# Optimization experiments

Hardware: AMD Instinct MI355X
Metric: run time of the kernel (lower is better)

The kernel has to match this reference:

```python
import jax, jax.numpy as jnp
import numpy as np

LAYERS, HIDDEN, FFN, HEADS = 2, 128, 256, 4
IMG_H, IMG_W = 32, 64
SEQ = IMG_H * IMG_W
HEAD = HIDDEN // HEADS          # 32, per-head qk dim
HEAD_V = 2 * HEAD               # double_v_dim=True
VDIM = HEADS * HEAD_V           # 256
B = 2
SCALE_BASE = 512.0
EPS = 1e-5


def _xpos_tables(seq, d):
    # XPOS: rotary angles + per-position exponential scale
    half = d // 2
    scale_vec = (jnp.arange(0, d, 2, dtype=jnp.float32) + 0.4 * d) / (1.4 * d)  # (d/2,)
    power = jnp.arange(seq, dtype=jnp.float32) / SCALE_BASE
    scale = scale_vec[None, :] ** power[:, None]                                 # (S, d/2)
    inv_freq = 1.0 / (10000.0 ** (jnp.arange(half, dtype=jnp.float32) / half))
    ang = jnp.arange(seq, dtype=jnp.float32)[:, None] * inv_freq[None, :]        # (S, d/2)
    return jnp.sin(ang), jnp.cos(ang), scale


def _apply_xpos(x, sin, cos, scale):
    # duplicate-interleave sin/cos*scale to width d, rotate-every-two
    s = jnp.repeat(sin * scale, 2, axis=-1)   # (S, d)
    c = jnp.repeat(cos * scale, 2, axis=-1)
    x1, x2 = x[..., ::2], x[..., 1::2]
    rot = jnp.stack([-x2, x1], axis=-1).reshape(x.shape)
    return x * c + rot * s


def _ln(x, g, b):
    mu = x.mean(-1, keepdims=True)
    var = ((x - mu) ** 2).mean(-1, keepdims=True)
    return (x - mu) * jax.lax.rsqrt(var + EPS) * g + b


def _gn(y, g, b):
    # GroupNorm(HEADS groups) over VDIM channels, applied per token
    bsz, s, v = y.shape
    yg = y.reshape(bsz, s, HEADS, HEAD_V)
    mu = yg.mean(-1, keepdims=True)
    var = ((yg - mu) ** 2).mean(-1, keepdims=True)
    yn = ((yg - mu) * jax.lax.rsqrt(var + EPS)).reshape(bsz, s, v)
    return yn * g + b


def _decay(seq):
    # D[h, n, m] = gamma_h^(n-m) for n >= m else 0
    gammas = 1.0 - jnp.exp(jnp.linspace(jnp.log(1.0 / 32.0), jnp.log(1.0 / 512.0), HEADS))
    n = jnp.arange(seq, dtype=jnp.float32)
    diff = n[:, None] - n[None, :]
    return (gammas[:, None, None] ** jnp.maximum(diff, 0.0)) * (diff >= 0.0)


def _forward(x, ln1_g, ln1_b, ln2_g, ln2_b, WQ, WK, WV, WG, WO, gn_g, gn_b, w1, b1, w2, b2):
    sin, cos, scale = _xpos_tables(SEQ, HEAD)
    D = _decay(SEQ)  # (H, S, S)
    for i in range(LAYERS):
        h = _ln(x, ln1_g[i], ln1_b[i])
        Q = _apply_xpos(jnp.einsum('bsd,hde->bhse', h, WQ[i]), sin, cos, scale)
        K = _apply_xpos(jnp.einsum('bsd,hde->bhse', h, WK[i]), sin, cos, 1.0 / scale)
        V = jnp.einsum('bsd,hdv->bhsv', h, WV[i])
        att = jnp.einsum('bhse,bhte->bhst', Q, K) * D[None]      # decay retention
        Y = jnp.einsum('bhst,bhtv->bhsv', att, V)
        Y = jnp.moveaxis(Y, 1, 2).reshape(x.shape[0], SEQ, VDIM)  # concat heads
        Y = _gn(Y, gn_g[i], gn_b[i])
        G = h @ WG[i]
        ret = (G * jax.nn.sigmoid(G) * Y) @ WO[i]                 # swish gate + out proj
        y = ret + x
        h2 = _ln(y, ln2_g[i], ln2_b[i])
        x = jax.nn.gelu(h2 @ w1[i] + b1[i], approximate=False) @ w2[i] + b2[i] + y
    return x.reshape(x.shape[0], IMG_H, IMG_W, x.shape[-1])


def setup_inputs() -> dict:
    key = jax.random.key(0)
    ks = jax.random.split(key, 8)
    def rn(k, shape, sc):
        return jax.random.normal(k, shape, dtype=jnp.float32) * sc
    s = 1.0 / np.sqrt(HIDDEN)
    return {
        'x': rn(ks[0], (B, SEQ, HIDDEN), 1.0),
        'ln1_g': jnp.ones((LAYERS, HIDDEN), jnp.float32),
        'ln1_b': jnp.zeros((LAYERS, HIDDEN), jnp.float32),
        'ln2_g': jnp.ones((LAYERS, HIDDEN), jnp.float32),
        'ln2_b': jnp.zeros((LAYERS, HIDDEN), jnp.float32),
        'WQ': rn(ks[1], (LAYERS, HEADS, HIDDEN, HEAD), s),
        'WK': rn(ks[2], (LAYERS, HEADS, HIDDEN, HEAD), s),
        'WV': rn(ks[3], (LAYERS, HEADS, HIDDEN, HEAD_V), s),
        'WG': rn(ks[4], (LAYERS, HIDDEN, VDIM), s),
        'WO': rn(ks[5], (LAYERS, VDIM, HIDDEN), 1.0 / np.sqrt(VDIM)),
        'gn_g': jnp.ones((LAYERS, VDIM), jnp.float32),
        'gn_b': jnp.zeros((LAYERS, VDIM), jnp.float32),
        'w1': rn(ks[6], (LAYERS, HIDDEN, FFN), s),
        'b1': jnp.zeros((LAYERS, FFN), jnp.float32),
        'w2': rn(ks[7], (LAYERS, FFN, HIDDEN), 1.0 / np.sqrt(FFN)),
        'b2': jnp.zeros((LAYERS, HIDDEN), jnp.float32),
    }


def reference(x, ln1_g, ln1_b, ln2_g, ln2_b, WQ, WK, WV, WG, WO, gn_g, gn_b, w1, b1, w2, b2):
    return _forward(x, ln1_g, ln1_b, ln2_g, ln2_b, WQ, WK, WV, WG, WO, gn_g, gn_b, w1, b1, w2, b2)
```

## Files before the change

kernel.cpp:

```cpp
#include <hip/hip_runtime.h>
#include <math.h>

#define NLAYERS 2
#define HID 128
#define FFND 256
#define NH 4
#define SEQL 2048
#define HD 32
#define HDV 64
#define VD 256
#define NBATCH 2
#define MROWS (NBATCH*SEQL)
#define NCAT 768
#define NCHUNK 32

__global__ __launch_bounds__(256) void setup_kernel(
    const float* __restrict__ WQ, const float* __restrict__ WK,
    const float* __restrict__ WV, const float* __restrict__ WG,
    float* __restrict__ Wcat, float* __restrict__ tabs)
{
  int bid = blockIdx.x;
  if (bid < 768) {
    int idx = bid * 256 + threadIdx.x;
    int l = idx / (HID * NCAT);
    int r = idx - l * (HID * NCAT);
    int k = r / NCAT;
    int n = r - k * NCAT;
    float v;
    if (n < 128)      { int h = n >> 5, e = n & 31;            v = WQ[(((l*NH+h)*HID)+k)*HD  + e]; }
    else if (n < 256) { int m = n-128; int h = m>>5, e = m&31; v = WK[(((l*NH+h)*HID)+k)*HD  + e]; }
    else if (n < 512) { int m = n-256; int h = m>>6, e = m&63; v = WV[(((l*NH+h)*HID)+k)*HDV + e]; }
    else              { v = WG[(l*HID + k)*VD + (n-512)]; }
    Wcat[idx] = v;
  } else {
    int idx = (bid - 768) * 256 + threadIdx.x;
    int s = idx >> 4, i = idx & 15;
    float inv_freq = powf(10000.f, -(float)i * (1.f/16.f));
    float ang = (float)s * inv_freq;
    float sv  = ((float)(2*i) + 0.4f*32.f) / (1.4f*32.f);
    float sc  = powf(sv, (float)s * (1.f/512.f));
    float sn = sinf(ang), cs = cosf(ang);
    tabs[idx]          = sn * sc;
    tabs[32768 + idx]  = cs * sc;
    tabs[65536 + idx]  = sn / sc;
    tabs[98304 + idx]  = cs / sc;
  }
}

template<bool XPOS, bool BIAS, bool GELU>
__global__ __launch_bounds__(512) void gemm_ln(
    const float* __restrict__ A, const float* __restrict__ Bw,
    const float* __restrict__ lng, const float* __restrict__ lnb,
    const float* __restrict__ bias, const float* __restrict__ tabs,
    float* __restrict__ C, int N)
{
  __shared__ float As[128][68];
  __shared__ float Bs[64][68];
  int tid = threadIdx.x;
  int tx2 = tid & 31, ty2 = tid >> 5;
  int rb = blockIdx.x * 64, nb = blockIdx.y * 64;

  {
    int row = tid >> 3, q = tid & 7;
    const float* ar = A + (size_t)(rb + row) * HID + 16 * q;
    float4 av[4];
    #pragma unroll
    for (int it = 0; it < 4; it++) av[it] = *(const float4*)(ar + 4*it);
    float s = 0.f;
    #pragma unroll
    for (int it = 0; it < 4; it++) s += av[it].x + av[it].y + av[it].z + av[it].w;
    s += __shfl_xor(s, 1); s += __shfl_xor(s, 2); s += __shfl_xor(s, 4);
    float mu = s * (1.f/128.f);
    float qs = 0.f;
    #pragma unroll
    for (int it = 0; it < 4; it++) {
      float d;
      d = av[it].x - mu; qs += d*d;  d = av[it].y - mu; qs += d*d;
      d = av[it].z - mu; qs += d*d;  d = av[it].w - mu; qs += d*d;
    }
    qs += __shfl_xor(qs, 1); qs += __shfl_xor(qs, 2); qs += __shfl_xor(qs, 4);
    float rs = rsqrtf(qs * (1.f/128.f) + 1e-5f);
    #pragma unroll
    for (int it = 0; it < 4; it++) {
      int k0 = 16*q + 4*it;
      float4 g4 = *(const float4*)(lng + k0);
      float4 b4 = *(const float4*)(lnb + k0);
      float vv[4] = { (av[it].x-mu)*rs*g4.x + b4.x, (av[it].y-mu)*rs*g4.y + b4.y,
                      (av[it].z-mu)*rs*g4.z + b4.z, (av[it].w-mu)*rs*g4.w + b4.w };
      #pragma unroll
      for (int d = 0; d < 4; d++) {
        int k = k0 + d;
        As[k][row ^ (4*((k>>2)&7)) ^ (16*((k>>5)&1))] = vv[d];
      }
    }
  }

  float acc[4][2];
  #pragma unroll
  for (int i=0;i<4;i++) { acc[i][0] = 0.f; acc[i][1] = 0.f; }

  for (int ks = 0; ks < 128; ks += 64) {
    #pragma unroll
    for (int it = 0; it < 2; it++) {
      int idx = it*512 + tid;
      int kk = idx >> 4, nq = idx & 15;
      *(float4*)(&Bs[kk][4*nq]) = *(const float4*)(Bw + (size_t)(ks+kk)*N + nb + 4*nq);
    }
    __syncthreads();
    #pragma unroll
    for (int kk = 0; kk < 64; kk++) {
      int k = ks + kk;
      float a[4];
      *(float4*)a = *(const float4*)&As[k][(4*ty2) ^ (4*((k>>2)&7)) ^ (16*((k>>5)&1))];
      float2 b2 = *(const float2*)&Bs[kk][2*tx2];
      #pragma unroll
      for (int i=0;i<4;i++) {
        acc[i][0] = fmaf(a[i], b2.x, acc[i][0]);
        acc[i][1] = fmaf(a[i], b2.y, acc[i][1]);
      }
    }
    __syncthreads();
  }

  #pragma unroll
  for (int i=0;i<4;i++) {
    int row = rb + 4*ty2 + i;
    int cb = nb + 2*tx2;
    float o[2];
    #pragma unroll
    for (int j=0;j<2;j++) {
      float v = acc[i][j];
      if (BIAS)  v += bias[cb + j];
      if (GELU)  v = 0.5f * v * (1.f + erff(v * 0.70710678118f));
      o[j] = v;
    }
    if (XPOS) {
      if (nb < 256) {
        bool isK = (nb >= 128);
        const float* sn_t = tabs + (isK ? 65536 : 0);
        const float* cs_t = tabs + (isK ? 98304 : 32768);
        int s = row & (SEQL - 1);
        int i0 = (cb & 31) >> 1;
        float sn = sn_t[s*16 + i0], cs = cs_t[s*16 + i0];
        float x1 = o[0], x2 = o[1];
        o[0] = x1*cs - x2*sn;  o[1] = x2*cs + x1*sn;
      }
    }
    *(float2*)(C + (size_t)row*N + cb) = *(float2*)o;
  }
}

template<bool BIAS>
__global__ __launch_bounds__(512) void gemm_n32(
    const float* __restrict__ A, const float* __restrict__ Bw,
    const float* __restrict__ bias, const float* __restrict__ Rsd,
    float* __restrict__ C, int N)
{
  __shared__ float As[64][68];
  __shared__ float Bs[64][36];
  int tid = threadIdx.x;
  int tx = tid & 15, ty = tid >> 4;
  int rb = blockIdx.x * 64, nb = blockIdx.y * 32;

  float acc[2][2];
  acc[0][0]=0.f; acc[0][1]=0.f; acc[1][0]=0.f; acc[1][1]=0.f;

  for (int ks = 0; ks < 256; ks += 64) {
    #pragma unroll
    for (int it = 0; it < 2; it++) {
      int idx = it*512 + tid;
      int row = idx >> 4, kq = idx & 15;
      float4 a4 = *(const float4*)(A + (size_t)(rb+row)*256 + ks + 4*kq);
      int rsw = row ^ (4*(kq & 7));
      As[4*kq+0][rsw] = a4.x; As[4*kq+1][rsw] = a4.y;
      As[4*kq+2][rsw] = a4.z; As[4*kq+3][rsw] = a4.w;
    }
    {
      int kk = tid >> 3, nq = tid & 7;
      *(float4*)(&Bs[kk][4*nq]) = *(const float4*)(Bw + (size_t)(ks+kk)*N + nb + 4*nq);
    }
    __syncthreads();
    #pragma unroll
    for (int k = 0; k < 64; k++) {
      float2 a2 = *(const float2*)&As[k][(2*ty) ^ (4*((k>>2)&7))];
      float2 b2 = *(const float2*)&Bs[k][2*tx];
      acc[0][0] = fmaf(a2.x, b2.x, acc[0][0]);
      acc[0][1] = fmaf(a2.x, b2.y, acc[0][1]);
      acc[1][0] = fmaf(a2.y, b2.x, acc[1][0]);
      acc[1][1] = fmaf(a2.y, b2.y, acc[1][1]);
    }
    __syncthreads();
  }

  #pragma unroll
  for (int i=0;i<2;i++) {
    int row = rb + 2*ty + i;
    int cb = nb + 2*tx;
    float o[2];
    #pragma unroll
    for (int j=0;j<2;j++) {
      float v = acc[i][j];
      if (BIAS) v += bias[cb + j];
      v += Rsd[(size_t)row*N + cb + j];
      o[j] = v;
    }
    *(float2*)(C + (size_t)row*N + cb) = *(float2*)o;
  }
}

__global__ __launch_bounds__(512) void ret_kv_kernel(
    const float* __restrict__ QKVG, float* __restrict__ Asum)
{
  int bh = blockIdx.x >> 5;
  int c  = blockIdx.x & 31;
  int b = bh >> 2, h = bh & 3;
  float t0 = logf(1.f/32.f) + (float)h * (logf(1.f/512.f) - logf(1.f/32.f)) * (1.f/3.f);
  float gamma = 1.f - expf(t0);
  float lg = logf(gamma);

  __shared__ float Ks[64][36];
  __shared__ float Vs[64][68];
  __shared__ float wt[64];

  int tid = threadIdx.x;
  int c0 = c * 64;
  const float* base = QKVG + (size_t)(b * SEQL) * NCAT;

  {
    int row = tid >> 3, eq = tid & 7;
    *(float4*)&Ks[row][4*eq] =
        *(const float4*)(base + (size_t)(c0+row)*NCAT + 128 + h*32 + 4*eq);
  }
  #pragma unroll
  for (int it = 0; it < 2; it++) {
    int idx = it*512 + tid;
    int row = idx >> 4, vq = idx & 15;
    *(float4*)&Vs[row][4*vq] =
        *(const float4*)(base + (size_t)(c0+row)*NCAT + 256 + h*64 + 4*vq);
  }
  if (tid < 64) wt[tid] = __expf(lg * (float)(64 - tid));
  __syncthreads();

  int e = tid >> 4, v4 = (tid & 15) * 4;
  float a0[4] = {0,0,0,0};
  #pragma unroll 8
  for (int t = 0; t < 64; t++) {
    float kw = Ks[t][e] * wt[t];
    float4 v0 = *(const float4*)&Vs[t][v4];
    a0[0] = fmaf(kw, v0.x, a0[0]); a0[1] = fmaf(kw, v0.y, a0[1]);
    a0[2] = fmaf(kw, v0.z, a0[2]); a0[3] = fmaf(kw, v0.w, a0[3]);
  }
  *(float4*)(Asum + ((size_t)(bh*NCHUNK + c))*2048 + e*64 + v4) = *(float4*)a0;
}

__global__ __launch_bounds__(512) void ret_out_kernel(
    const float* __restrict__ QKVG, const float* __restrict__ Asum,
    const float* __restrict__ gn_g, const float* __restrict__ gn_b,
    float* __restrict__ Gated)
{
  int bh = blockIdx.x >> 5;
  int c  = blockIdx.x & 31;
  int b = bh >> 2, h = bh & 3;
  float t0 = logf(1.f/32.f) + (float)h * (logf(1.f/512.f) - logf(1.f/32.f)) * (1.f/3.f);
  float gamma = 1.f - expf(t0);
  float lg = logf(gamma);
  float g64 = __expf(lg * 64.f);

  __shared__ float Qs[64][36];
  __shared__ float Ks[64][36];
  __shared__ float Vs[64][68];
  __shared__ float Ss[64][68];
  __shared__ float Sc[32][68];

  int tid = threadIdx.x;
  int tx2 = tid & 31, ty2 = tid >> 5;
  int c0 = c * 64;
  const float* base = QKVG + (size_t)(b * SEQL) * NCAT;

  {
    int row = tid >> 3, eq = tid & 7;
    *(float4*)&Qs[row][4*eq] =
        *(const float4*)(base + (size_t)(c0+row)*NCAT + h*32 + 4*eq);
    int esw = (4*eq) ^ (4*((row >> 2) & 7));
    *(float4*)&Ks[row][esw] =
        *(const float4*)(base + (size_t)(c0+row)*NCAT + 128 + h*32 + 4*eq);
  }
  #pragma unroll
  for (int it = 0; it < 2; it++) {
    int idx = it*512 + tid;
    int row = idx >> 4, vq = idx & 15;
    *(float4*)&Vs[row][4*vq] =
        *(const float4*)(base + (size_t)(c0+row)*NCAT + 256 + h*64 + 4*vq);
  }

  {
    int e = tid >> 4, v4 = (tid & 15) * 4;
    float s0[4] = {0,0,0,0};
    float w = 1.f;
    const float* ab = Asum + ((size_t)bh*NCHUNK)*2048 + e*64 + v4;
    for (int cp = c-1; cp >= 0; --cp) {
      const float* ap = ab + (size_t)cp*2048;
      float4 x0 = *(const float4*)ap;
      s0[0] = fmaf(w, x0.x, s0[0]); s0[1] = fmaf(w, x0.y, s0[1]);
      s0[2] = fmaf(w, x0.z, s0[2]); s0[3] = fmaf(w, x0.w, s0[3]);
      w *= g64;
    }
    *(float4*)&Sc[e][v4] = *(float4*)s0;
  }
  __syncthreads();

  float sacc[4][2];
  #pragma unroll
  for (int i=0;i<4;i++) { sacc[i][0]=0.f; sacc[i][1]=0.f; }
  #pragma unroll
  for (int e = 0; e < 32; e += 4) {
    float qv[4][4], kv[2][4];
    #pragma unroll
    for (int i=0;i<4;i++)
      *(float4*)qv[i] = *(const float4*)&Qs[4*ty2+i][e];
    #pragma unroll
    for (int j=0;j<2;j++) {
      int kr = 2*tx2 + j;
      *(float4*)kv[j] = *(const float4*)&Ks[kr][e ^ (4*((kr>>2)&7))];
    }
    #pragma unroll
    for (int i=0;i<4;i++)
      #pragma unroll
      for (int j=0;j<2;j++)
        sacc[i][j] = fmaf(qv[i][0], kv[j][0],
                     fmaf(qv[i][1], kv[j][1],
                     fmaf(qv[i][2], kv[j][2],
                     fmaf(qv[i][3], kv[j][3], sacc[i][j]))));
  }
  #pragma unroll
  for (int i=0;i<4;i++) {
    int sl = 4*ty2 + i;
    float o2[2];
    #pragma unroll
    for (int j=0;j<2;j++) {
      int dr = sl - (2*tx2 + j);
      float w = (dr >= 0) ? __expf(lg * (float)dr) : 0.f;
      o2[j] = sacc[i][j] * w;
    }
    *(float2*)&Ss[sl][2*tx2] = *(float2*)o2;
  }

  float acc[4][2];
  #pragma unroll
  for (int i=0;i<4;i++) { acc[i][0]=0.f; acc[i][1]=0.f; }
  #pragma unroll
  for (int e = 0; e < 32; e += 4) {
    float qv[4][4], sv[4][2];
    #pragma unroll
    for (int i=0;i<4;i++)
      *(float4*)qv[i] = *(const float4*)&Qs[4*ty2+i][e];
    #pragma unroll
    for (int m=0;m<4;m++)
      *(float2*)sv[m] = *(const float2*)&Sc[e+m][2*tx2];
    #pragma unroll
    for (int i=0;i<4;i++)
      #pragma unroll
      for (int j=0;j<2;j++)
        acc[i][j] = fmaf(qv[i][0], sv[0][j],
                    fmaf(qv[i][1], sv[1][j],
                    fmaf(qv[i][2], sv[2][j],
                    fmaf(qv[i][3], sv[3][j], acc[i][j]))));
  }
  #pragma unroll
  for (int i=0;i<4;i++) {
    float gr = __expf(lg * (float)(4*ty2 + i));
    acc[i][0] *= gr; acc[i][1] *= gr;
  }
  __syncthreads();

  #pragma unroll
  for (int t = 0; t < 64; t += 4) {
    float sv[4][4], vv[4][2];
    #pragma unroll
    for (int i=0;i<4;i++)
      *(float4*)sv[i] = *(const float4*)&Ss[4*ty2+i][t];
    #pragma unroll
    for (int m=0;m<4;m++)
      *(float2*)vv[m] = *(const float2*)&Vs[t+m][2*tx2];
    #pragma unroll
    for (int i=0;i<4;i++)
      #pragma unroll
      for (int j=0;j<2;j++)
        acc[i][j] = fmaf(sv[i][0], vv[0][j],
                    fmaf(sv[i][1], vv[1][j],
                    fmaf(sv[i][2], vv[2][j],
                    fmaf(sv[i][3], vv[3][j], acc[i][j]))));
  }

  #pragma unroll
  for (int i=0;i<4;i++) {
    float s1 = acc[i][0] + acc[i][1];
    #pragma unroll
    for (int o = 16; o; o >>= 1) s1 += __shfl_xor(s1, o);
    float mu = s1 * (1.f/64.f);
    float q = 0.f;
    #pragma unroll
    for (int j=0;j<2;j++) { float d = acc[i][j] - mu; q += d*d; }
    #pragma unroll
    for (int o = 16; o; o >>= 1) q += __shfl_xor(q, o);
    float rs = rsqrtf(q * (1.f/64.f) + 1e-5f);
    int row = b*SEQL + c0 + 4*ty2 + i;
    float2 g2 = *(const float2*)(QKVG + (size_t)row*NCAT + 512 + h*64 + 2*tx2);
    float gv[2] = {g2.x, g2.y};
    float o2[2];
    #pragma unroll
    for (int j=0;j<2;j++) {
      int col = h*64 + 2*tx2 + j;
      float yn = (acc[i][j] - mu) * rs * gn_g[col] + gn_b[col];
      float g = gv[j];
      float sig = 1.f / (1.f + __expf(-g));
      o2[j] = g * sig * yn;
    }
    *(float2*)(Gated + (size_t)row*VD + h*64 + 2*tx2) = *(float2*)o2;
  }
}

extern "C" void kernel_launch(void* const* d_in, const int* in_sizes, int n_in,
                              void* d_out, int out_size, void* d_ws, size_t ws_size,
                              hipStream_t stream)
{
  (void)in_sizes; (void)n_in; (void)out_size; (void)ws_size;
  const float* x_in  = (const float*)d_in[0];
  const float* ln1_g = (const float*)d_in[1];
  const float* ln1_b = (const float*)d_in[2];
  const float* ln2_g = (const float*)d_in[3];
  const float* ln2_b = (const float*)d_in[4];
  const float* WQ    = (const float*)d_in[5];
  const float* WK    = (const float*)d_in[6];
  const float* WV    = (const float*)d_in[7];
  const float* WG    = (const float*)d_in[8];
  const float* WO    = (const float*)d_in[9];
  const float* gn_g  = (const float*)d_in[10];
  const float* gn_b  = (const float*)d_in[11];
  const float* w1    = (const float*)d_in[12];
  const float* b1    = (const float*)d_in[13];
  const float* w2    = (const float*)d_in[14];
  const float* b2    = (const float*)d_in[15];
  float* out = (float*)d_out;
  float* ws  = (float*)d_ws;

  float* Wcat = ws;
  float* tabs = Wcat + 196608;
  float* QKVG = tabs + 131072;
  float* Asum = QKVG + 3145728;
  float* Gt   = Asum + 524288;
  float* Yres = Gt   + 1048576;
  float* Mid  = Yres + 524288;

  setup_kernel<<<896, 256, 0, stream>>>(WQ, WK, WV, WG, Wcat, tabs);

  for (int l = 0; l < NLAYERS; l++) {
    const float* xl = (l == 0) ? x_in : out;
    gemm_ln<true,false,false><<<dim3(MROWS/64, NCAT/64), 512, 0, stream>>>(
        xl, Wcat + l*HID*NCAT, ln1_g + l*HID, ln1_b + l*HID,
        nullptr, tabs, QKVG, NCAT);
    ret_kv_kernel<<<256, 512, 0, stream>>>(QKVG, Asum);
    ret_out_kernel<<<256, 512, 0, stream>>>(QKVG, Asum, gn_g + l*VD, gn_b + l*VD, Gt);
    gemm_n32<false><<<dim3(MROWS/64, HID/32), 512, 0, stream>>>(
        Gt, WO + l*VD*HID, nullptr, xl, Yres, HID);
    gemm_ln<false,true,true><<<dim3(MROWS/64, FFND/64), 512, 0, stream>>>(
        Yres, w1 + l*HID*FFND, ln2_g + l*HID, ln2_b + l*HID,
        b1 + l*FFND, nullptr, Mid, FFND);
    gemm_n32<true><<<dim3(MROWS/64, HID/32), 512, 0, stream>>>(
        Mid, w2 + l*FFND*HID, b2 + l*HID, Yres, out, HID);
  }
}
```

Before: 232.5 us.

## Fuse LN+QKVG projection with chunk KV state and fuse whole FFN block

Replaces the setup kernel, the LN+QKVG GEMM and the separate KV-state kernel with one kernel. It reads the weights directly, computes the xPos tables inline, and emits partial per-16-row KV sums that ret_out now adds up four at a time. The WO projection, residual add, LN2, W1 with GELU, W2 and the second residual are merged into a single kernel over 16-row tiles. This cuts kernel launches from 13 to 6 and avoids round trips through global memory for intermediates. In exchange, each block reads the weights directly from global memory with no shared-memory tiling, and only 256 blocks are launched.

Measured after the change: 287.5 us. +23.6%, slower.

```diff
diff --git a/kernel.cpp b/kernel.cpp
--- a/kernel.cpp
+++ b/kernel.cpp
@@ -14,256 +14,180 @@
 #define NCAT 768
 #define NCHUNK 32
 
-__global__ __launch_bounds__(256) void setup_kernel(
+#define LG32   (-3.4657359028f)
+#define DLT    (-0.9241962407f)
+__device__ __forceinline__ float lgamma_h(int h) {
+  return logf(1.f - expf(LG32 + DLT * (float)h));
+}
+
+__global__ __launch_bounds__(512) void fuse_qkvg(
+    const float* __restrict__ X,
+    const float* __restrict__ lng, const float* __restrict__ lnb,
     const float* __restrict__ WQ, const float* __restrict__ WK,
     const float* __restrict__ WV, const float* __restrict__ WG,
-    float* __restrict__ Wcat, float* __restrict__ tabs)
+    float* __restrict__ QKVG, float* __restrict__ Asum4, int l)
 {
-  int bid = blockIdx.x;
-  if (bid < 768) {
-    int idx = bid * 256 + threadIdx.x;
-    int l = idx / (HID * NCAT);
-    int r = idx - l * (HID * NCAT);
-    int k = r / NCAT;
-    int n = r - k * NCAT;
-    float v;
-    if (n < 128)      { int h = n >> 5, e = n & 31;            v = WQ[(((l*NH+h)*HID)+k)*HD  + e]; }
-    else if (n < 256) { int m = n-128; int h = m>>5, e = m&31; v = WK[(((l*NH+h)*HID)+k)*HD  + e]; }
-    else if (n < 512) { int m = n-256; int h = m>>6, e = m&63; v = WV[(((l*NH+h)*HID)+k)*HDV + e]; }
-    else              { v = WG[(l*HID + k)*VD + (n-512)]; }
-    Wcat[idx] = v;
-  } else {
-    int idx = (bid - 768) * 256 + threadIdx.x;
-    int s = idx >> 4, i = idx & 15;
-    float inv_freq = powf(10000.f, -(float)i * (1.f/16.f));
-    float ang = (float)s * inv_freq;
-    float sv  = ((float)(2*i) + 0.4f*32.f) / (1.4f*32.f);
-    float sc  = powf(sv, (float)s * (1.f/512.f));
-    float sn = sinf(ang), cs = cosf(ang);
-    tabs[idx]          = sn * sc;
-    tabs[32768 + idx]  = cs * sc;
-    tabs[65536 + idx]  = sn / sc;
-    tabs[98304 + idx]  = cs / sc;
+  __shared__ union {
+    float As[128][20];
+    struct { float wK[16][132]; float Vl[16][260]; } kv;
+  } sm;
+
+  int tid = threadIdx.x;
+  int rb = blockIdx.x * 16;
+  int ty = tid >> 6;
+  int tx = tid & 63;
+
+  {
+    int row = tid >> 5, q = tid & 31;
+    float4 av = *(const float4*)(X + (size_t)(rb + row) * HID + 4*q);
+    float s = av.x + av.y + av.z + av.w;
+    s += __shfl_xor(s, 1);  s += __shfl_xor(s, 2);
+    s += __shfl_xor(s, 4);  s += __shfl_xor(s, 8);  s += __shfl_xor(s, 16);
+    float mu = s * (1.f/128.f);
+    float dx = av.x-mu, dy = av.y-mu, dz = av.z-mu, dw = av.w-mu;
+    float qs = dx*dx + dy*dy + dz*dz + dw*dw;
+    qs += __shfl_xor(qs, 1);  qs += __shfl_xor(qs, 2);
+    qs += __shfl_xor(qs, 4);  qs += __shfl_xor(qs, 8);  qs += __shfl_xor(qs, 16);
+    float rs = rsqrtf(qs * (1.f/128.f) + 1e-5f);
+    float4 g4 = *(const float4*)(lng + 4*q);
+    float4 b4 = *(const float4*)(lnb + 4*q);
+    sm.As[4*q+0][row] = dx*rs*g4.x + b4.x;
+    sm.As[4*q+1][row] = dy*rs*g4.y + b4.y;
+    sm.As[4*q+2][row] = dz*rs*g4.z + b4.z;
+    sm.As[4*q+3][row] = dw*rs*g4.w + b4.w;
+  }
+
+  bool isK = (tx >= 32);
+  int txk = isK ? (tx - 32) : tx;
+  int cq  = 4 * txk;
+  const float* b0 = (isK ? WK : WQ) + (size_t)l*NH*HID*HD
+                    + (txk >> 3) * (HID*HD) + (cq & 31);
+  const float* b1 = WV + (size_t)l*NH*HID*HDV
+                    + (tx >> 4) * (HID*HDV) + ((4*tx) & 63);
+  const float* b2 = WG + (size_t)l*HID*VD + 4*tx;
+
+  __syncthreads();
+
+  float acc[2][12];
+  #pragma unroll
+  for (int i=0;i<2;i++)
+    #pragma unroll
+    for (int j=0;j<12;j++) acc[i][j] = 0.f;
+
+  #pragma unroll 4
+  for (int k = 0; k < 128; k++) {
+    float2 a = *(const float2*)&sm.As[k][2*ty];
+    float4 q0 = *(const float4*)(b0 + k*HD);
+    float4 v0 = *(const float4*)(b1 + k*HDV);
+    float4 g0 = *(const float4*)(b2 + k*VD);
+    float bv[12] = { q0.x,q0.y,q0.z,q0.w, v0.x,v0.y,v0.z,v0.w, g0.x,g0.y,g0.z,g0.w };
+    float ar[2] = { a.x, a.y };
+    #pragma unroll
+    for (int i=0;i<2;i++)
+      #pragma unroll
+      for (int j=0;j<12;j++)
+        acc[i][j] = fmaf(ar[i], bv[j], acc[i][j]);
+  }
+
+  {
+    float sgn = isK ? -1.f : 1.f;
+    #pragma unroll
+    for (int P = 0; P < 2; P++) {
+      float fi   = (float)(((cq & 31) >> 1) + P);
+      float invf = exp2f(fi * -0.83048202372f);
+      float sv   = (2.f*fi + 12.8f) * (1.f/44.8f);
+      float l2sv = log2f(sv) * (1.f/512.f) * sgn;
+      #pragma unroll
+      for (int i=0;i<2;i++) {
+        float s  = (float)((rb & (SEQL-1)) + 2*ty + i);
+        float ang = s * invf;
+        float sc  = exp2f(l2sv * s);
+        float sn = sinf(ang) * sc, cs = cosf(ang) * sc;
+        float x1 = acc[i][2*P], x2 = acc[i][2*P+1];
+        acc[i][2*P]   = x1*cs - x2*sn;
+        acc[i][2*P+1] = x2*cs + x1*sn;
+      }
+    }
+  }
+
+  #pragma unroll
+  for (int i=0;i<2;i++) {
+    float* cp = QKVG + (size_t)(rb + 2*ty + i) * NCAT;
+    float o0[4] = {acc[i][0],acc[i][1],acc[i][2],acc[i][3]};
+    float o1[4] = {acc[i][4],acc[i][5],acc[i][6],acc[i][7]};
+    float o2[4] = {acc[i][8],acc[i][9],acc[i][10],acc[i][11]};
+    *(float4*)(cp + 4*tx)       = *(float4*)o0;
+    *(float4*)(cp + 256 + 4*tx) = *(float4*)o1;
+    *(float4*)(cp + 512 + 4*tx) = *(float4*)o2;
+  }
+
+  __syncthreads();
+
+  if (isK) {
+    float lgk = lgamma_h(cq >> 5);
+    #pragma unroll
+    for (int i=0;i<2;i++) {
+      int t = 2*ty + i;
+      float w = expf(lgk * (float)(16 - t));
+      float o[4] = {acc[i][0]*w, acc[i][1]*w, acc[i][2]*w, acc[i][3]*w};
+      *(float4*)&sm.kv.wK[t][cq] = *(float4*)o;
+    }
+  }
+  #pragma unroll
+  for (int i=0;i<2;i++) {
+    float o[4] = {acc[i][4],acc[i][5],acc[i][6],acc[i][7]};
+    *(float4*)&sm.kv.Vl[2*ty+i][4*tx] = *(float4*)o;
+  }
+  __syncthreads();
+
+  {
+    int h  = tid >> 7;
+    int u  = tid & 127;
+    int e2 = u >> 3;
+    int v8 = u & 7;
+    float pa[2][8];
+    #pragma unroll
+    for (int i=0;i<2;i++)
+      #pragma unroll
+      for (int j=0;j<8;j++) pa[i][j] = 0.f;
+    #pragma unroll
+    for (int t = 0; t < 16; t++) {
+      float2 ke = *(const float2*)&sm.kv.wK[t][h*32 + 2*e2];
+      float4 va = *(const float4*)&sm.kv.Vl[t][h*64 + 8*v8];
+      float4 vb = *(const float4*)&sm.kv.Vl[t][h*64 + 8*v8 + 4];
+      float vv[8] = {va.x,va.y,va.z,va.w, vb.x,vb.y,vb.z,vb.w};
+      float kk[2] = {ke.x, ke.y};
+      #pragma unroll
+      for (int i=0;i<2;i++)
+        #pragma unroll
+        for (int j=0;j<8;j++)
+          pa[i][j] = fmaf(kk[i], vv[j], pa[i][j]);
+    }
+    int b = rb >> 11;
+    int c = (rb & (SEQL-1)) >> 6;
+    int p = (rb >> 4) & 3;
+    float scale = expf(lgamma_h(h) * (float)(48 - 16*p));
+    float* ob = Asum4 + ((size_t)((b*NH + h)*NCHUNK + c)*4 + p)*2048
+                + (2*e2)*64 + 8*v8;
+    #pragma unroll
+    for (int i=0;i<2;i++) {
+      float o0[4] = {pa[i][0]*scale, pa[i][1]*scale, pa[i][2]*scale, pa[i][3]*scale};
+      float o1[4] = {pa[i][4]*scale, pa[i][5]*scale, pa[i][6]*scale, pa[i][7]*scale};
+      *(float4*)(ob + i*64)     = *(float4*)o0;
+      *(float4*)(ob + i*64 + 4) = *(float4*)o1;
+    }
   }
 }
 
-template<bool XPOS, bool BIAS, bool GELU>
-__global__ __launch_bounds__(512) void gemm_ln(
-    const float* __restrict__ A, const float* __restrict__ Bw,
-    const float* __restrict__ lng, const float* __restrict__ lnb,
-    const float* __restrict__ bias, const float* __restrict__ tabs,
-    float* __restrict__ C, int N)
-{
-  __shared__ float As[128][68];
-  __shared__ float Bs[64][68];
-  int tid = threadIdx.x;
-  int tx2 = tid & 31, ty2 = tid >> 5;
-  int rb = blockIdx.x * 64, nb = blockIdx.y * 64;
-
-  {
-    int row = tid >> 3, q = tid & 7;
-    const float* ar = A + (size_t)(rb + row) * HID + 16 * q;
-    float4 av[4];
-    #pragma unroll
-    for (int it = 0; it < 4; it++) av[it] = *(const float4*)(ar + 4*it);
-    float s = 0.f;
-    #pragma unroll
-    for (int it = 0; it < 4; it++) s += av[it].x + av[it].y + av[it].z + av[it].w;
-    s += __shfl_xor(s, 1); s += __shfl_xor(s, 2); s += __shfl_xor(s, 4);
-    float mu = s * (1.f/128.f);
-    float qs = 0.f;
-    #pragma unroll
-    for (int it = 0; it < 4; it++) {
-      float d;
-      d = av[it].x - mu; qs += d*d;  d = av[it].y - mu; qs += d*d;
-      d = av[it].z - mu; qs += d*d;  d = av[it].w - mu; qs += d*d;
-    }
-    qs += __shfl_xor(qs, 1); qs += __shfl_xor(qs, 2); qs += __shfl_xor(qs, 4);
-    float rs = rsqrtf(qs * (1.f/128.f) + 1e-5f);
-    #pragma unroll
-    for (int it = 0; it < 4; it++) {
-      int k0 = 16*q + 4*it;
-      float4 g4 = *(const float4*)(lng + k0);
-      float4 b4 = *(const float4*)(lnb + k0);
-      float vv[4] = { (av[it].x-mu)*rs*g4.x + b4.x, (av[it].y-mu)*rs*g4.y + b4.y,
-                      (av[it].z-mu)*rs*g4.z + b4.z, (av[it].w-mu)*rs*g4.w + b4.w };
-      #pragma unroll
-      for (int d = 0; d < 4; d++) {
-        int k = k0 + d;
-        As[k][row ^ (4*((k>>2)&7)) ^ (16*((k>>5)&1))] = vv[d];
-      }
-    }
-  }
-
-  float acc[4][2];
-  #pragma unroll
-  for (int i=0;i<4;i++) { acc[i][0] = 0.f; acc[i][1] = 0.f; }
-
-  for (int ks = 0; ks < 128; ks += 64) {
-    #pragma unroll
-    for (int it = 0; it < 2; it++) {
-      int idx = it*512 + tid;
-      int kk = idx >> 4, nq = idx & 15;
-      *(float4*)(&Bs[kk][4*nq]) = *(const float4*)(Bw + (size_t)(ks+kk)*N + nb + 4*nq);
-    }
-    __syncthreads();
-    #pragma unroll
-    for (int kk = 0; kk < 64; kk++) {
-      int k = ks + kk;
-      float a[4];
-      *(float4*)a = *(const float4*)&As[k][(4*ty2) ^ (4*((k>>2)&7)) ^ (16*((k>>5)&1))];
-      float2 b2 = *(const float2*)&Bs[kk][2*tx2];
-      #pragma unroll
-      for (int i=0;i<4;i++) {
-        acc[i][0] = fmaf(a[i], b2.x, acc[i][0]);
-        acc[i][1] = fmaf(a[i], b2.y, acc[i][1]);
-      }
-    }
-    __syncthreads();
-  }
-
-  #pragma unroll
-  for (int i=0;i<4;i++) {
-    int row = rb + 4*ty2 + i;
-    int cb = nb + 2*tx2;
-    float o[2];
-    #pragma unroll
-    for (int j=0;j<2;j++) {
-      float v = acc[i][j];
-      if (BIAS)  v += bias[cb + j];
-      if (GELU)  v = 0.5f * v * (1.f + erff(v * 0.70710678118f));
-      o[j] = v;
-    }
-    if (XPOS) {
-      if (nb < 256) {
-        bool isK = (nb >= 128);
-        const float* sn_t = tabs + (isK ? 65536 : 0);
-        const float* cs_t = tabs + (isK ? 98304 : 32768);
-        int s = row & (SEQL - 1);
-        int i0 = (cb & 31) >> 1;
-        float sn = sn_t[s*16 + i0], cs = cs_t[s*16 + i0];
-        float x1 = o[0], x2 = o[1];
-        o[0] = x1*cs - x2*sn;  o[1] = x2*cs + x1*sn;
-      }
-    }
-    *(float2*)(C + (size_t)row*N + cb) = *(float2*)o;
-  }
-}
-
-template<bool BIAS>
-__global__ __launch_bounds__(512) void gemm_n32(
-    const float* __restrict__ A, const float* __restrict__ Bw,
-    const float* __restrict__ bias, const float* __restrict__ Rsd,
-    float* __restrict__ C, int N)
-{
-  __shared__ float As[64][68];
-  __shared__ float Bs[64][36];
-  int tid = threadIdx.x;
-  int tx = tid & 15, ty = tid >> 4;
-  int rb = blockIdx.x * 64, nb = blockIdx.y * 32;
-
-  float acc[2][2];
-  acc[0][0]=0.f; acc[0][1]=0.f; acc[1][0]=0.f; acc[1][1]=0.f;
-
-  for (int ks = 0; ks < 256; ks += 64) {
-    #pragma unroll
-    for (int it = 0; it < 2; it++) {
-      int idx = it*512 + tid;
-      int row = idx >> 4, kq = idx & 15;
-      float4 a4 = *(const float4*)(A + (size_t)(rb+row)*256 + ks + 4*kq);
-      int rsw = row ^ (4*(kq & 7));
-      As[4*kq+0][rsw] = a4.x; As[4*kq+1][rsw] = a4.y;
-      As[4*kq+2][rsw] = a4.z; As[4*kq+3][rsw] = a4.w;
-    }
-    {
-      int kk = tid >> 3, nq = tid & 7;
-      *(float4*)(&Bs[kk][4*nq]) = *(const float4*)(Bw + (size_t)(ks+kk)*N + nb + 4*nq);
-    }
-    __syncthreads();
-    #pragma unroll
-    for (int k = 0; k < 64; k++) {
-      float2 a2 = *(const float2*)&As[k][(2*ty) ^ (4*((k>>2)&7))];
-      float2 b2 = *(const float2*)&Bs[k][2*tx];
-      acc[0][0] = fmaf(a2.x, b2.x, acc[0][0]);
-      acc[0][1] = fmaf(a2.x, b2.y, acc[0][1]);
-      acc[1][0] = fmaf(a2.y, b2.x, acc[1][0]);
-      acc[1][1] = fmaf(a2.y, b2.y, acc[1][1]);
-    }
-    __syncthreads();
-  }
-
-  #pragma unroll
-  for (int i=0;i<2;i++) {
-    int row = rb + 2*ty + i;
-    int cb = nb + 2*tx;
-    float o[2];
-    #pragma unroll
-    for (int j=0;j<2;j++) {
-      float v = acc[i][j];
-      if (BIAS) v += bias[cb + j];
-      v += Rsd[(size_t)row*N + cb + j];
-      o[j] = v;
-    }
-    *(float2*)(C + (size_t)row*N + cb) = *(float2*)o;
-  }
-}
-
-__global__ __launch_bounds__(512) void ret_kv_kernel(
-    const float* __restrict__ QKVG, float* __restrict__ Asum)
-{
-  int bh = blockIdx.x >> 5;
-  int c  = blockIdx.x & 31;
-  int b = bh >> 2, h = bh & 3;
-  float t0 = logf(1.f/32.f) + (float)h * (logf(1.f/512.f) - logf(1.f/32.f)) * (1.f/3.f);
-  float gamma = 1.f - expf(t0);
-  float lg = logf(gamma);
-
-  __shared__ float Ks[64][36];
-  __shared__ float Vs[64][68];
-  __shared__ float wt[64];
-
-  int tid = threadIdx.x;
-  int c0 = c * 64;
-  const float* base = QKVG + (size_t)(b * SEQL) * NCAT;
-
-  {
-    int row = tid >> 3, eq = tid & 7;
-    *(float4*)&Ks[row][4*eq] =
-        *(const float4*)(base + (size_t)(c0+row)*NCAT + 128 + h*32 + 4*eq);
-  }
-  #pragma unroll
-  for (int it = 0; it < 2; it++) {
-    int idx = it*512 + tid;
-    int row = idx >> 4, vq = idx & 15;
-    *(float4*)&Vs[row][4*vq] =
-        *(const float4*)(base + (size_t)(c0+row)*NCAT + 256 + h*64 + 4*vq);
-  }
-  if (tid < 64) wt[tid] = __expf(lg * (float)(64 - tid));
-  __syncthreads();
-
-  int e = tid >> 4, v4 = (tid & 15) * 4;
-  float a0[4] = {0,0,0,0};
-  #pragma unroll 8
-  for (int t = 0; t < 64; t++) {
-    float kw = Ks[t][e] * wt[t];
-    float4 v0 = *(const float4*)&Vs[t][v4];
-    a0[0] = fmaf(kw, v0.x, a0[0]); a0[1] = fmaf(kw, v0.y, a0[1]);
-    a0[2] = fmaf(kw, v0.z, a0[2]); a0[3] = fmaf(kw, v0.w, a0[3]);
-  }
-  *(float4*)(Asum + ((size_t)(bh*NCHUNK + c))*2048 + e*64 + v4) = *(float4*)a0;
-}
-
 __global__ __launch_bounds__(512) void ret_out_kernel(
-    const float* __restrict__ QKVG, const float* __restrict__ Asum,
+    const float* __restrict__ QKVG, const float* __restrict__ Asum4,
     const float* __restrict__ gn_g, const float* __restrict__ gn_b,
     float* __restrict__ Gated)
 {
   int bh = blockIdx.x >> 5;
   int c  = blockIdx.x & 31;
   int b = bh >> 2, h = bh & 3;
-  float t0 = logf(1.f/32.f) + (float)h * (logf(1.f/512.f) - logf(1.f/32.f)) * (1.f/3.f);
-  float gamma = 1.f - expf(t0);
-  float lg = logf(gamma);
+  float lg = lgamma_h(h);
   float g64 = __expf(lg * 64.f);
 
   __shared__ float Qs[64][36];
@@ -297,12 +221,17 @@
     int e = tid >> 4, v4 = (tid & 15) * 4;
     float s0[4] = {0,0,0,0};
     float w = 1.f;
-    const float* ab = Asum + ((size_t)bh*NCHUNK)*2048 + e*64 + v4;
+    const float* ab = Asum4 + ((size_t)bh*NCHUNK*4)*2048 + e*64 + v4;
     for (int cp = c-1; cp >= 0; --cp) {
-      const float* ap = ab + (size_t)cp*2048;
+      const float* ap = ab + (size_t)cp*4*2048;
       float4 x0 = *(const float4*)ap;
-      s0[0] = fmaf(w, x0.x, s0[0]); s0[1] = fmaf(w, x0.y, s0[1]);
-      s0[2] = fmaf(w, x0.z, s0[2]); s0[3] = fmaf(w, x0.w, s0[3]);
+      float4 x1 = *(const float4*)(ap + 2048);
+      float4 x2 = *(const float4*)(ap + 4096);
+      float4 x3 = *(const float4*)(ap + 6144);
+      float sx = x0.x+x1.x+x2.x+x3.x, sy = x0.y+x1.y+x2.y+x3.y;
+      float sz = x0.z+x1.z+x2.z+x3.z, sw = x0.w+x1.w+x2.w+x3.w;
+      s0[0] = fmaf(w, sx, s0[0]); s0[1] = fmaf(w, sy, s0[1]);
+      s0[2] = fmaf(w, sz, s0[2]); s0[3] = fmaf(w, sw, s0[3]);
       w *= g64;
     }
     *(float4*)&Sc[e][v4] = *(float4*)s0;
@@ -417,6 +346,123 @@
       o2[j] = g * sig * yn;
     }
     *(float2*)(Gated + (size_t)row*VD + h*64 + 2*tx2) = *(float2*)o2;
+  }
+}
+
+__global__ __launch_bounds__(512) void fuse_ffn(
+    const float* __restrict__ Gated, const float* __restrict__ WO,
+    const float* __restrict__ Xres,
+    const float* __restrict__ lng, const float* __restrict__ lnb,
+    const float* __restrict__ w1, const float* __restrict__ b1,
+    const float* __restrict__ w2, const float* __restrict__ b2,
+    float* __restrict__ Out)
+{
+  __shared__ float bufA[256][20];
+  __shared__ float h2s[128][20];
+  __shared__ float Ys[16][130];
+
+  int tid = threadIdx.x;
+  int rb = blockIdx.x * 16;
+  int ty = tid >> 6;
+  int tx = tid & 63;
+
+  {
+    int row = tid >> 5, q = tid & 31;
+    const float* gr = Gated + (size_t)(rb + row) * VD + 8*q;
+    float4 a0 = *(const float4*)gr;
+    float4 a1 = *(const float4*)(gr + 4);
+    bufA[8*q+0][row] = a0.x; bufA[8*q+1][row] = a0.y;
+    bufA[8*q+2][row] = a0.z; bufA[8*q+3][row] = a0.w;
+    bufA[8*q+4][row] = a1.x; bufA[8*q+5][row] = a1.y;
+    bufA[8*q+6][row] = a1.z; bufA[8*q+7][row] = a1.w;
+  }
+  __syncthreads();
+
+  float yr[2][2];
+  {
+    float acc[2][2] = {{0.f,0.f},{0.f,0.f}};
+    #pragma unroll 8
+    for (int k = 0; k < 256; k++) {
+      float2 a = *(const float2*)&bufA[k][2*ty];
+      float2 bb = *(const float2*)(WO + (size_t)k*HID + 2*tx);
+      acc[0][0] = fmaf(a.x, bb.x, acc[0][0]);
+      acc[0][1] = fmaf(a.x, bb.y, acc[0][1]);
+      acc[1][0] = fmaf(a.y, bb.x, acc[1][0]);
+      acc[1][1] = fmaf(a.y, bb.y, acc[1][1]);
+    }
+    #pragma unroll
+    for (int i=0;i<2;i++) {
+      float2 xr = *(const float2*)(Xres + (size_t)(rb + 2*ty + i)*HID + 2*tx);
+      yr[i][0] = acc[i][0] + xr.x;
+      yr[i][1] = acc[i][1] + xr.y;
+    }
+  }
+
+  #pragma unroll
+  for (int i=0;i<2;i++) {
+    float s = yr[i][0] + yr[i][1];
+    #pragma unroll
+    for (int o = 32; o; o >>= 1) s += __shfl_xor(s, o);
+    float mu = s * (1.f/128.f);
+    float d0 = yr[i][0]-mu, d1 = yr[i][1]-mu;
+    float q = d0*d0 + d1*d1;
+    #pragma unroll
+    for (int o = 32; o; o >>= 1) q += __shfl_xor(q, o);
+    float rs = rsqrtf(q * (1.f/128.f) + 1e-5f);
+    h2s[2*tx+0][2*ty+i] = d0*rs*lng[2*tx+0] + lnb[2*tx+0];
+    h2s[2*tx+1][2*ty+i] = d1*rs*lng[2*tx+1] + lnb[2*tx+1];
+    float o2[2] = {yr[i][0], yr[i][1]};
+    *(float2*)&Ys[2*ty+i][2*tx] = *(float2*)o2;
+  }
+  __syncthreads();
+
+  {
+    float acc[2][4];
+    #pragma unroll
+    for (int i=0;i<2;i++)
+      #pragma unroll
+      for (int j=0;j<4;j++) acc[i][j] = 0.f;
+    #pragma unroll 8
+    for (int k = 0; k < 128; k++) {
+      float2 a = *(const float2*)&h2s[k][2*ty];
+      float4 bb = *(const float4*)(w1 + (size_t)k*FFND + 4*tx);
+      float bv[4] = {bb.x,bb.y,bb.z,bb.w};
+      #pragma unroll
+      for (int j=0;j<4;j++) {
+        acc[0][j] = fmaf(a.x, bv[j], acc[0][j]);
+        acc[1][j] = fmaf(a.y, bv[j], acc[1][j]);
+      }
+    }
+    float4 bi = *(const float4*)(b1 + 4*tx);
+    float bvi[4] = {bi.x,bi.y,bi.z,bi.w};
+    #pragma unroll
+    for (int i=0;i<2;i++)
+      #pragma unroll
+      for (int j=0;j<4;j++) {
+        float v = acc[i][j] + bvi[j];
+        bufA[4*tx+j][2*ty+i] = 0.5f * v * (1.f + erff(v * 0.70710678118f));
+      }
+  }
+  __syncthreads();
+
+  {
+    float acc[2][2] = {{0.f,0.f},{0.f,0.f}};
+    #pragma unroll 8
+    for (int k = 0; k < 256; k++) {
+      float2 a = *(const float2*)&bufA[k][2*ty];
+      float2 bb = *(const float2*)(w2 + (size_t)k*HID + 2*tx);
+      acc[0][0] = fmaf(a.x, bb.x, acc[0][0]);
+      acc[0][1] = fmaf(a.x, bb.y, acc[0][1]);
+      acc[1][0] = fmaf(a.y, bb.x, acc[1][0]);
+      acc[1][1] = fmaf(a.y, bb.y, acc[1][1]);
+    }
+    #pragma unroll
+    for (int i=0;i<2;i++) {
+      float2 yv = *(const float2*)&Ys[2*ty+i][2*tx];
+      float o2[2] = { acc[i][0] + b2[2*tx+0] + yv.x,
+                      acc[i][1] + b2[2*tx+1] + yv.y };
+      *(float2*)(Out + (size_t)(rb + 2*ty + i)*HID + 2*tx) = *(float2*)o2;
+    }
   }
 }
 
@@ -444,29 +490,18 @@
   float* out = (float*)d_out;
   float* ws  = (float*)d_ws;
 
-  float* Wcat = ws;
-  float* tabs = Wcat + 196608;
-  float* QKVG = tabs + 131072;
-  float* Asum = QKVG + 3145728;
-  float* Gt   = Asum + 524288;
-  float* Yres = Gt   + 1048576;
-  float* Mid  = Yres + 524288;
-
-  setup_kernel<<<896, 256, 0, stream>>>(WQ, WK, WV, WG, Wcat, tabs);
+  float* QKVG  = ws;
+  float* Asum4 = QKVG + 3145728;
+  float* Gt    = Asum4 + 2097152;
 
   for (int l = 0; l < NLAYERS; l++) {
     const float* xl = (l == 0) ? x_in : out;
-    gemm_ln<true,false,false><<<dim3(MROWS/64, NCAT/64), 512, 0, stream>>>(
-        xl, Wcat + l*HID*NCAT, ln1_g + l*HID, ln1_b + l*HID,
-        nullptr, tabs, QKVG, NCAT);
-    ret_kv_kernel<<<256, 512, 0, stream>>>(QKVG, Asum);
-    ret_out_kernel<<<256, 512, 0, stream>>>(QKVG, Asum, gn_g + l*VD, gn_b + l*VD, Gt);
-    gemm_n32<false><<<dim3(MROWS/64, HID/32), 512, 0, stream>>>(
-        Gt, WO + l*VD*HID, nullptr, xl, Yres, HID);
-    gemm_ln<false,true,true><<<dim3(MROWS/64, FFND/64), 512, 0, stream>>>(
-        Yres, w1 + l*HID*FFND, ln2_g + l*HID, ln2_b + l*HID,
-        b1 + l*FFND, nullptr, Mid, FFND);
-    gemm_n32<true><<<dim3(MROWS/64, HID/32), 512, 0, stream>>>(
-        Mid, w2 + l*FFND*HID, b2 + l*HID, Yres, out, HID);
+    fuse_qkvg<<<256, 512, 0, stream>>>(
+        xl, ln1_g + l*HID, ln1_b + l*HID, WQ, WK, WV, WG, QKVG, Asum4, l);
+    ret_out_kernel<<<256, 512, 0, stream>>>(
+        QKVG, Asum4, gn_g + l*VD, gn_b + l*VD, Gt);
+    fuse_ffn<<<256, 512, 0, stream>>>(
+        Gt, WO + l*VD*HID, xl, ln2_g + l*HID, ln2_b + l*HID,
+        w1 + l*HID*FFND, b1 + l*FFND, w2 + l*FFND*HID, b2 + l*HID, out);
   }
 }
```
